# Kernel tuning notes

Hardware: AMD Instinct MI355X
Metric: run time of the kernel (lower is better)

The kernel has to match this reference:

```python
import jax, jax.numpy as jnp
import numpy as np

NS = 100000
H = 128  # embedding_dim
K = 4    # heads


def setup_inputs() -> dict:
    key = jax.random.key(0)
    ks = jax.random.split(key, 8)
    return {
        "e": jax.random.normal(ks[0], (NS, H), dtype=jnp.float32),
        "w_key": jax.random.normal(ks[1], (K, 1), dtype=jnp.float32),
        "w_value": jax.random.normal(ks[2], (K, 1), dtype=jnp.float32),
        "q": jax.random.normal(ks[3], (H,), dtype=jnp.float32),
        "mu_w": jax.random.normal(ks[4], (1, H), dtype=jnp.float32) * (1.0 / np.sqrt(H)),
        "mu_b": jax.random.normal(ks[5], (1,), dtype=jnp.float32) * 0.01,
        "sigma_w": jax.random.normal(ks[6], (1, H), dtype=jnp.float32) * (1.0 / np.sqrt(H)),
        "sigma_b": jax.random.normal(ks[7], (1,), dtype=jnp.float32) * 0.01,
    }


def reference(e, w_key, w_value, q, mu_w, mu_b, sigma_w, sigma_b):
    # e: [Ns, H] -> unsqueeze(0) -> [1, Ns, H]
    e3 = e[None, :, :]
    # w_key/w_value: [K, 1]; einsum 'kd,dnh->knh' -> [K, Ns, H]
    k = jnp.einsum('kd,dnh->knh', w_key, e3)
    v = jnp.einsum('kd,dnh->knh', w_value, e3)
    # L2-normalized attention logits: [K, Ns]
    q_norm = jnp.linalg.norm(q)                    # scalar
    k_norm = jnp.linalg.norm(k, axis=-1)           # [K, Ns]
    a_att = jnp.einsum('h,knh->kn', q, k) / (q_norm * k_norm)
    a_att = jnp.maximum(a_att, 0.0)
    a_att = a_att / jnp.maximum(jnp.sum(a_att, axis=-1, keepdims=True), 1e-6)
    # weighted aggregation over stocks: [K, H]
    h_multi = jnp.einsum('kn,knh->kh', a_att, v)
    # linear heads -> [K]
    mu_z = jnp.squeeze(h_multi @ mu_w.T + mu_b, axis=-1)
    sigma_z = jax.nn.softplus(jnp.squeeze(h_multi @ sigma_w.T + sigma_b, axis=-1))
    return (mu_z, sigma_z)
```

## Files before the change

kernel.cpp:

```cpp
#include <hip/hip_runtime.h>
#include <math.h>

#define NS 100000
#define H 128
#define NHEADS 4
#define NPAIRS (NS / 2)
#define BATCH 4
#define NB (NPAIRS / BATCH)
#define TPB 256
#define NBLK 1024
#define NREP 8

__device__ __forceinline__ float dot4(float4 a, float4 b) {
    return a.x * b.x + a.y * b.y + a.z * b.z + a.w * b.w;
}

__device__ __forceinline__ void fma4(float4& acc, float w, float4 v) {
    acc.x = fmaf(w, v.x, acc.x); acc.y = fmaf(w, v.y, acc.y);
    acc.z = fmaf(w, v.z, acc.z); acc.w = fmaf(w, v.w, acc.w);
}

__global__ __launch_bounds__(TPB) void fp_pass1(const float* __restrict__ e,
                                                const float* __restrict__ q,
                                                float* __restrict__ g) {
    const int tid  = threadIdx.x;
    const int lane = tid & 63;
    const int widx = tid >> 6;
    const int half = lane >> 5;
    const int c4   = (lane & 31) << 2;

    const float4 q4 = *(const float4*)(q + c4);
    float qn = dot4(q4, q4);
    qn += __shfl_xor(qn, 1);  qn += __shfl_xor(qn, 2);  qn += __shfl_xor(qn, 4);
    qn += __shfl_xor(qn, 8);  qn += __shfl_xor(qn, 16);
    const float inv_qn = rsqrtf(qn);

    float4 up = {0.f, 0.f, 0.f, 0.f};
    float4 um = {0.f, 0.f, 0.f, 0.f};
    float sp = 0.f, sm = 0.f;

    const int gw = blockIdx.x * (TPB / 64) + widx;
    const int W  = NBLK * (TPB / 64);

    const float* base = e + (size_t)half * H + c4;

    float4 v0, v1, v2, v3;
    float4 n0 = {0,0,0,0}, n1 = {0,0,0,0}, n2 = {0,0,0,0}, n3 = {0,0,0,0};
    int b = gw;
    if (b < NB) {
        const float* p = base + (size_t)b * (8 * H);
        v0 = *(const float4*)(p);
        v1 = *(const float4*)(p + 2 * H);
        v2 = *(const float4*)(p + 4 * H);
        v3 = *(const float4*)(p + 6 * H);
    }
    while (b < NB) {
        const int bn = b + W;
        if (bn < NB) {
            const float* p = base + (size_t)bn * (8 * H);
            n0 = *(const float4*)(p);
            n1 = *(const float4*)(p + 2 * H);
            n2 = *(const float4*)(p + 4 * H);
            n3 = *(const float4*)(p + 6 * H);
        }
        float d0 = dot4(v0, q4), d1 = dot4(v1, q4), d2 = dot4(v2, q4), d3 = dot4(v3, q4);
        float s0 = dot4(v0, v0), s1 = dot4(v1, v1), s2 = dot4(v2, v2), s3 = dot4(v3, v3);
#define LVL(m)                                                        \
        d0 += __shfl_xor(d0, m); d1 += __shfl_xor(d1, m);             \
        d2 += __shfl_xor(d2, m); d3 += __shfl_xor(d3, m);             \
        s0 += __shfl_xor(s0, m); s1 += __shfl_xor(s1, m);             \
        s2 += __shfl_xor(s2, m); s3 += __shfl_xor(s3, m);
        LVL(1) LVL(2) LVL(4) LVL(8) LVL(16)
#undef LVL
        const float c0 = d0 * rsqrtf(s0) * inv_qn;
        const float c1 = d1 * rsqrtf(s1) * inv_qn;
        const float c2 = d2 * rsqrtf(s2) * inv_qn;
        const float c3 = d3 * rsqrtf(s3) * inv_qn;
        const float wp0 = fmaxf(c0, 0.f), wm0 = fmaxf(-c0, 0.f);
        const float wp1 = fmaxf(c1, 0.f), wm1 = fmaxf(-c1, 0.f);
        const float wp2 = fmaxf(c2, 0.f), wm2 = fmaxf(-c2, 0.f);
        const float wp3 = fmaxf(c3, 0.f), wm3 = fmaxf(-c3, 0.f);
        sp += (wp0 + wp1) + (wp2 + wp3);
        sm += (wm0 + wm1) + (wm2 + wm3);
        fma4(up, wp0, v0); fma4(up, wp1, v1); fma4(up, wp2, v2); fma4(up, wp3, v3);
        fma4(um, wm0, v0); fma4(um, wm1, v1); fma4(um, wm2, v2); fma4(um, wm3, v3);
        v0 = n0; v1 = n1; v2 = n2; v3 = n3;
        b = bn;
    }

    __shared__ float s_up[8][H];
    __shared__ float s_um[8][H];
    __shared__ float s_s[8][2];
    const int hs = widx * 2 + half;
    *(float4*)(&s_up[hs][c4]) = up;
    *(float4*)(&s_um[hs][c4]) = um;
    if ((lane & 31) == 0) {
        s_s[hs][0] = sp;
        s_s[hs][1] = sm;
    }
    __syncthreads();

    float* gr = g + (blockIdx.x & (NREP - 1)) * 258;
    if (tid < H) {
        float a = 0.f;
#pragma unroll
        for (int h2 = 0; h2 < 8; ++h2) a += s_up[h2][tid];
        atomicAdd(&gr[tid], a);
    } else {
        const int t = tid - H;
        float a = 0.f;
#pragma unroll
        for (int h2 = 0; h2 < 8; ++h2) a += s_um[h2][t];
        atomicAdd(&gr[H + t], a);
    }
    if (tid < 2) {
        float a = 0.f;
#pragma unroll
        for (int h2 = 0; h2 < 8; ++h2) a += s_s[h2][tid];
        atomicAdd(&gr[256 + tid], a);
    }
}

__global__ __launch_bounds__(256) void fp_finalize(const float* __restrict__ g,
                                                   const float* __restrict__ w_key,
                                                   const float* __restrict__ w_value,
                                                   const float* __restrict__ mu_w,
                                                   const float* __restrict__ mu_b,
                                                   const float* __restrict__ sigma_w,
                                                   const float* __restrict__ sigma_b,
                                                   float* __restrict__ out) {
    __shared__ float tot[258];
    const int tid = threadIdx.x;
    {
        float a = 0.f;
#pragma unroll
        for (int r = 0; r < NREP; ++r) a += g[r * 258 + tid];
        tot[tid] = a;
    }
    if (tid < 2) {
        float a = 0.f;
#pragma unroll
        for (int r = 0; r < NREP; ++r) a += g[r * 258 + 256 + tid];
        tot[256 + tid] = a;
    }
    __syncthreads();

    if (tid < 64) {
        const int l = tid;
        const float up0 = tot[2 * l], up1 = tot[2 * l + 1];
        const float um0 = tot[H + 2 * l], um1 = tot[H + 2 * l + 1];
        const float mw0 = mu_w[2 * l], mw1 = mu_w[2 * l + 1];
        const float sw0 = sigma_w[2 * l], sw1 = sigma_w[2 * l + 1];
        float A = up0 * mw0 + up1 * mw1;
        float B = up0 * sw0 + up1 * sw1;
        float C = um0 * mw0 + um1 * mw1;
        float D = um0 * sw0 + um1 * sw1;
#pragma unroll
        for (int m = 1; m < 64; m <<= 1) {
            A += __shfl_xor(A, m);
            B += __shfl_xor(B, m);
            C += __shfl_xor(C, m);
            D += __shfl_xor(D, m);
        }
        if (l < NHEADS) {
            const float spv = fmaxf(tot[256], 1e-6f);
            const float smv = fmaxf(tot[257], 1e-6f);
            const float wk = w_key[l];
            const float wv = w_value[l];
            float dmu, dsg;
            if (wk > 0.f) {
                dmu = A / spv; dsg = B / spv;
            } else if (wk < 0.f) {
                dmu = C / smv; dsg = D / smv;
            } else {
                dmu = 0.f; dsg = 0.f;
            }
            out[l] = fmaf(wv, dmu, mu_b[0]);
            const float x = fmaf(wv, dsg, sigma_b[0]);
            out[NHEADS + l] = fmaxf(x, 0.f) + log1pf(expf(-fabsf(x)));
        }
    }
}

extern "C" void kernel_launch(void* const* d_in, const int* in_sizes, int n_in,
                              void* d_out, int out_size, void* d_ws, size_t ws_size,
                              hipStream_t stream) {
    const float* e       = (const float*)d_in[0];
    const float* w_key   = (const float*)d_in[1];
    const float* w_value = (const float*)d_in[2];
    const float* q       = (const float*)d_in[3];
    const float* mu_w    = (const float*)d_in[4];
    const float* mu_b    = (const float*)d_in[5];
    const float* sigma_w = (const float*)d_in[6];
    const float* sigma_b = (const float*)d_in[7];
    float* out = (float*)d_out;
    float* g   = (float*)d_ws;

    hipLaunchKernelGGL(fp_pass1, dim3(NBLK), dim3(TPB), 0, stream, e, q, g);
    hipLaunchKernelGGL(fp_finalize, dim3(1), dim3(256), 0, stream, g,
                       w_key, w_value, mu_w, mu_b, sigma_w, sigma_b, out);
}
```

Baseline: 101.1 us.

## Assign one batch per wave with a full grid and more reduction replicas

Replaces the grid-stride loop with software prefetch by a launch of 3125 blocks, where each wave processes exactly one 8-row batch. All loads are issued up front and occupancy is raised via launch bounds. This is meant to increase memory-level parallelism and hide DRAM latency better. The cost is about three times as many global atomics, spread over 32 replicas instead of 8, and it relies on the workspace being large enough and zeroed.

```diff
diff --git a/kernel.cpp b/kernel.cpp
--- a/kernel.cpp
+++ b/kernel.cpp
@@ -4,12 +4,9 @@
 #define NS 100000
 #define H 128
 #define NHEADS 4
-#define NPAIRS (NS / 2)
-#define BATCH 4
-#define NB (NPAIRS / BATCH)
 #define TPB 256
-#define NBLK 1024
-#define NREP 8
+#define NBLK 3125
+#define NREP 32
 
 __device__ __forceinline__ float dot4(float4 a, float4 b) {
     return a.x * b.x + a.y * b.y + a.z * b.z + a.w * b.w;
@@ -20,14 +17,21 @@
     acc.z = fmaf(w, v.z, acc.z); acc.w = fmaf(w, v.w, acc.w);
 }
 
-__global__ __launch_bounds__(TPB) void fp_pass1(const float* __restrict__ e,
-                                                const float* __restrict__ q,
-                                                float* __restrict__ g) {
+__global__ __launch_bounds__(TPB, 8) void fp_pass1(const float* __restrict__ e,
+                                                   const float* __restrict__ q,
+                                                   float* __restrict__ g) {
     const int tid  = threadIdx.x;
     const int lane = tid & 63;
     const int widx = tid >> 6;
     const int half = lane >> 5;
     const int c4   = (lane & 31) << 2;
+
+    const int gw = blockIdx.x * (TPB / 64) + widx;
+    const float* p = e + (size_t)gw * (8 * H) + (size_t)half * H + c4;
+    const float4 v0 = *(const float4*)(p);
+    const float4 v1 = *(const float4*)(p + 2 * H);
+    const float4 v2 = *(const float4*)(p + 4 * H);
+    const float4 v3 = *(const float4*)(p + 6 * H);
 
     const float4 q4 = *(const float4*)(q + c4);
     float qn = dot4(q4, q4);
@@ -35,58 +39,29 @@
     qn += __shfl_xor(qn, 8);  qn += __shfl_xor(qn, 16);
     const float inv_qn = rsqrtf(qn);
 
+    float d0 = dot4(v0, q4), d1 = dot4(v1, q4), d2 = dot4(v2, q4), d3 = dot4(v3, q4);
+    float s0 = dot4(v0, v0), s1 = dot4(v1, v1), s2 = dot4(v2, v2), s3 = dot4(v3, v3);
+#define LVL(m)                                                        \
+    d0 += __shfl_xor(d0, m); d1 += __shfl_xor(d1, m);                 \
+    d2 += __shfl_xor(d2, m); d3 += __shfl_xor(d3, m);                 \
+    s0 += __shfl_xor(s0, m); s1 += __shfl_xor(s1, m);                 \
+    s2 += __shfl_xor(s2, m); s3 += __shfl_xor(s3, m);
+    LVL(1) LVL(2) LVL(4) LVL(8) LVL(16)
+#undef LVL
+    const float c0 = d0 * rsqrtf(s0) * inv_qn;
+    const float c1 = d1 * rsqrtf(s1) * inv_qn;
+    const float c2 = d2 * rsqrtf(s2) * inv_qn;
+    const float c3 = d3 * rsqrtf(s3) * inv_qn;
+    const float wp0 = fmaxf(c0, 0.f), wm0 = fmaxf(-c0, 0.f);
+    const float wp1 = fmaxf(c1, 0.f), wm1 = fmaxf(-c1, 0.f);
+    const float wp2 = fmaxf(c2, 0.f), wm2 = fmaxf(-c2, 0.f);
+    const float wp3 = fmaxf(c3, 0.f), wm3 = fmaxf(-c3, 0.f);
+    const float sp = (wp0 + wp1) + (wp2 + wp3);
+    const float sm = (wm0 + wm1) + (wm2 + wm3);
     float4 up = {0.f, 0.f, 0.f, 0.f};
     float4 um = {0.f, 0.f, 0.f, 0.f};
-    float sp = 0.f, sm = 0.f;
-
-    const int gw = blockIdx.x * (TPB / 64) + widx;
-    const int W  = NBLK * (TPB / 64);
-
-    const float* base = e + (size_t)half * H + c4;
-
-    float4 v0, v1, v2, v3;
-    float4 n0 = {0,0,0,0}, n1 = {0,0,0,0}, n2 = {0,0,0,0}, n3 = {0,0,0,0};
-    int b = gw;
-    if (b < NB) {
-        const float* p = base + (size_t)b * (8 * H);
-        v0 = *(const float4*)(p);
-        v1 = *(const float4*)(p + 2 * H);
-        v2 = *(const float4*)(p + 4 * H);
-        v3 = *(const float4*)(p + 6 * H);
-    }
-    while (b < NB) {
-        const int bn = b + W;
-        if (bn < NB) {
-            const float* p = base + (size_t)bn * (8 * H);
-            n0 = *(const float4*)(p);
-            n1 = *(const float4*)(p + 2 * H);
-            n2 = *(const float4*)(p + 4 * H);
-            n3 = *(const float4*)(p + 6 * H);
-        }
-        float d0 = dot4(v0, q4), d1 = dot4(v1, q4), d2 = dot4(v2, q4), d3 = dot4(v3, q4);
-        float s0 = dot4(v0, v0), s1 = dot4(v1, v1), s2 = dot4(v2, v2), s3 = dot4(v3, v3);
-#define LVL(m)                                                        \
-        d0 += __shfl_xor(d0, m); d1 += __shfl_xor(d1, m);             \
-        d2 += __shfl_xor(d2, m); d3 += __shfl_xor(d3, m);             \
-        s0 += __shfl_xor(s0, m); s1 += __shfl_xor(s1, m);             \
-        s2 += __shfl_xor(s2, m); s3 += __shfl_xor(s3, m);
-        LVL(1) LVL(2) LVL(4) LVL(8) LVL(16)
-#undef LVL
-        const float c0 = d0 * rsqrtf(s0) * inv_qn;
-        const float c1 = d1 * rsqrtf(s1) * inv_qn;
-        const float c2 = d2 * rsqrtf(s2) * inv_qn;
-        const float c3 = d3 * rsqrtf(s3) * inv_qn;
-        const float wp0 = fmaxf(c0, 0.f), wm0 = fmaxf(-c0, 0.f);
-        const float wp1 = fmaxf(c1, 0.f), wm1 = fmaxf(-c1, 0.f);
-        const float wp2 = fmaxf(c2, 0.f), wm2 = fmaxf(-c2, 0.f);
-        const float wp3 = fmaxf(c3, 0.f), wm3 = fmaxf(-c3, 0.f);
-        sp += (wp0 + wp1) + (wp2 + wp3);
-        sm += (wm0 + wm1) + (wm2 + wm3);
-        fma4(up, wp0, v0); fma4(up, wp1, v1); fma4(up, wp2, v2); fma4(up, wp3, v3);
-        fma4(um, wm0, v0); fma4(um, wm1, v1); fma4(um, wm2, v2); fma4(um, wm3, v3);
-        v0 = n0; v1 = n1; v2 = n2; v3 = n3;
-        b = bn;
-    }
+    fma4(up, wp0, v0); fma4(up, wp1, v1); fma4(up, wp2, v2); fma4(up, wp3, v3);
+    fma4(um, wm0, v0); fma4(um, wm1, v1); fma4(um, wm2, v2); fma4(um, wm3, v3);
 
     __shared__ float s_up[8][H];
     __shared__ float s_um[8][H];
```

Result: faster. 98.42 us (-2.6%).
